# Kernel tuning notes

Hardware: AMD Instinct MI355X
Metric: run time of the kernel (lower is better)

## Reference

```python
import jax, jax.numpy as jnp
import numpy as np

N, B, OBS, ACT = 8, 32768, 128, 32
E, H = 128, 4
D = E // H  # attend_dim = 32
EPS = 1e-5


def setup_inputs() -> dict:
    key = jax.random.key(0)
    ks = jax.random.split(key, 20)
    sc = np.float32(0.02)
    inp = {
        "observation_vector": jax.random.normal(ks[0], (N, B, OBS), jnp.float32),
        "action_vector": jax.random.normal(ks[1], (N, B, ACT), jnp.float32),
        # per-agent BatchNorm affine params (training-mode batch stats are used)
        "bn_g_gamma": jnp.ones((N, OBS + ACT), jnp.float32),
        "bn_g_beta": jnp.zeros((N, OBS + ACT), jnp.float32),
        "bn_s_gamma": jnp.ones((N, OBS), jnp.float32),
        "bn_s_beta": jnp.zeros((N, OBS), jnp.float32),
        # per-agent g / state-only Linear layers
        "g_w": jax.random.normal(ks[2], (N, E, OBS + ACT), jnp.float32) * sc,
        "g_b": jnp.zeros((N, E), jnp.float32),
        "s_w": jax.random.normal(ks[3], (N, E, OBS), jnp.float32) * sc,
        "s_b": jnp.zeros((N, E), jnp.float32),
        # per-head attention projections (no bias)
        "wq": jax.random.normal(ks[4], (H, D, E), jnp.float32) * sc,
        "wk": jax.random.normal(ks[5], (H, D, E), jnp.float32) * sc,
        "wv": jax.random.normal(ks[6], (H, D, E), jnp.float32) * sc,
        # per-agent f networks: Linear(E + H*D -> E), Linear(E -> ACT)
        "f1_w": jax.random.normal(ks[7], (N, E, E + H * D), jnp.float32) * sc,
        "f1_b": jnp.zeros((N, E), jnp.float32),
        "f2_w": jax.random.normal(ks[8], (N, ACT, E), jnp.float32) * sc,
        "f2_b": jnp.zeros((N, ACT), jnp.float32),
    }
    return inp


def _bn(x, gamma, beta):
    # x: [N, B, F]; training-mode BatchNorm1d per agent (biased variance)
    mu = x.mean(axis=1, keepdims=True)
    var = x.var(axis=1, keepdims=True)
    return (x - mu) / jnp.sqrt(var + EPS) * gamma[:, None, :] + beta[:, None, :]


def _lrelu(x):
    return jax.nn.leaky_relu(x, 0.01)


def reference(observation_vector, action_vector, bn_g_gamma, bn_g_beta, bn_s_gamma,
              bn_s_beta, g_w, g_b, s_w, s_b, wq, wk, wv, f1_w, f1_b, f2_w, f2_b):
    obs, act = observation_vector, action_vector
    ga = jnp.concatenate([obs, act], axis=-1)                       # [N,B,OBS+ACT]
    e = _lrelu(jnp.einsum('nbf,nef->nbe', _bn(ga, bn_g_gamma, bn_g_beta), g_w)
               + g_b[:, None, :])                                   # [N,B,E]
    s = _lrelu(jnp.einsum('nbf,nef->nbe', _bn(obs, bn_s_gamma, bn_s_beta), s_w)
               + s_b[:, None, :])                                   # [N,B,E]
    q = jnp.einsum('nbe,hde->hnbd', e, wq)                          # [H,N,B,D]
    k = jnp.einsum('nbe,hde->hnbd', e, wk)
    v = _lrelu(jnp.einsum('nbe,hde->hnbd', e, wv))
    # leave-one-out attention over agents: mask the diagonal (self)
    logits = jnp.einsum('hnbd,hmbd->hbnm', q, k) / jnp.sqrt(jnp.float32(D))
    logits = jnp.where(jnp.eye(N, dtype=bool), -jnp.inf, logits)
    alpha = jax.nn.softmax(logits, axis=-1)                         # [H,B,N,N]
    xi = jnp.einsum('hbnm,hmbd->nbhd', alpha, v)                    # [N,B,H,D]
    xi = xi.reshape(N, xi.shape[1], H * D)
    fin = jnp.concatenate([xi, s], axis=-1)                         # [N,B,H*D+E]
    h1 = _lrelu(jnp.einsum('nbf,nef->nbe', fin, f1_w) + f1_b[:, None, :])
    all_q = jnp.einsum('nbe,nae->nba', h1, f2_w) + f2_b[:, None, :]  # [N,B,ACT]
    ids = jnp.argmax(act, axis=-1, keepdims=True)                   # [N,B,1]
    curr_q = jnp.take_along_axis(all_q, ids, axis=-1)               # [N,B,1]
    return curr_q
```

## Files before the change

### kernel.cpp

```cpp
#include <hip/hip_runtime.h>

#define N_AG 8
#define BTOT 32768
#define OBSF 128
#define ACTF 32
#define HH 4

#define WS_STATS   0u
#define WS_SCALES  (16u<<10)
#define WS_BIASES  (48u<<10)
#define WS_WQKV    (64u<<10)
#define WS_F2W     (160u<<10)
#define WS_F1W     (224u<<10)
#define WS_WG      (768u<<10)
#define WS_IDS     (1536u<<10)
#define WS_ES      (4u<<20)
#define WS_XI      (136u<<20)
#define WS_NEED    ((size_t)200<<20)

typedef __attribute__((ext_vector_type(8))) __bf16 bf16x8;
typedef __attribute__((ext_vector_type(8))) short short8;
typedef __attribute__((ext_vector_type(4))) float f32x4;

static __device__ __forceinline__ unsigned short f2bf(float f){
  unsigned u = __builtin_bit_cast(unsigned, f);
  u += 0x7fffu + ((u >> 16) & 1u);
  return (unsigned short)(u >> 16);
}
static __device__ __forceinline__ bf16x8 ldb8(const unsigned short* p){
  return __builtin_bit_cast(bf16x8, *(const short8*)p);
}
static __device__ __forceinline__ f32x4 mfma16(bf16x8 a, bf16x8 b, f32x4 c){
  return __builtin_amdgcn_mfma_f32_16x16x32_bf16(a, b, c, 0, 0, 0);
}

__global__ void k_zero(float* stats){
  for (int i = threadIdx.x; i < 2560; i += 256) stats[i] = 0.f;
}

__global__ __launch_bounds__(256) void k_stats_obs(const float* __restrict__ obs,
                                                   float* __restrict__ stats){
  int n = blockIdx.y, ch = blockIdx.x;
  int c = threadIdx.x & 31, r = threadIdx.x >> 5;
  const float4* p = (const float4*)(obs + ((size_t)n*BTOT + (size_t)ch*256 + r)*OBSF) + c;
  float sx=0.f, sy=0.f, sz=0.f, sw=0.f;
  float qx=0.f, qy=0.f, qz=0.f, qw=0.f;
  #pragma unroll 4
  for (int i = 0; i < 32; i++){
    float4 v = p[(size_t)i*8*(OBSF/4)];
    sx += v.x; sy += v.y; sz += v.z; sw += v.w;
    qx += v.x*v.x; qy += v.y*v.y; qz += v.z*v.z; qw += v.w*v.w;
  }
  __shared__ float4 rs[8][32], rq[8][32];
  rs[r][c] = make_float4(sx, sy, sz, sw);
  rq[r][c] = make_float4(qx, qy, qz, qw);
  __syncthreads();
  if (threadIdx.x < 128){
    int f = threadIdx.x;
    float ss = 0.f, qq = 0.f;
    #pragma unroll
    for (int g = 0; g < 8; g++){
      ss += ((const float*)&rs[g][f>>2])[f&3];
      qq += ((const float*)&rq[g][f>>2])[f&3];
    }
    atomicAdd(&stats[n*128 + f], ss);
    atomicAdd(&stats[1024 + n*128 + f], qq);
  }
}

__global__ __launch_bounds__(256) void k_stats_act(const float* __restrict__ act,
                                                   float* __restrict__ stats,
                                                   int* __restrict__ ids){
  int n = blockIdx.y, ch = blockIdx.x;
  int c = threadIdx.x & 7, r = threadIdx.x >> 3;
  int f0 = c*4;
  float sx=0.f, sy=0.f, sz=0.f, sw=0.f;
  float qx=0.f, qy=0.f, qz=0.f, qw=0.f;
  #pragma unroll
  for (int i = 0; i < 4; i++){
    int b = ch*128 + i*32 + r;
    float4 v = *(const float4*)(act + ((size_t)n*BTOT + b)*ACTF + f0);
    sx += v.x; sy += v.y; sz += v.z; sw += v.w;
    qx += v.x*v.x; qy += v.y*v.y; qz += v.z*v.z; qw += v.w*v.w;
    float mv = v.x; int mi = f0;
    if (v.y > mv){ mv = v.y; mi = f0+1; }
    if (v.z > mv){ mv = v.z; mi = f0+2; }
    if (v.w > mv){ mv = v.w; mi = f0+3; }
    #pragma unroll
    for (int m = 1; m <= 4; m <<= 1){
      float ov = __shfl_xor(mv, m);
      int   oi = __shfl_xor(mi, m);
      if (ov > mv || (ov == mv && oi < mi)){ mv = ov; mi = oi; }
    }
    if (c == 0) ids[(size_t)n*BTOT + b] = mi;
  }
  __shared__ float4 rs[32][8], rq[32][8];
  rs[r][c] = make_float4(sx, sy, sz, sw);
  rq[r][c] = make_float4(qx, qy, qz, qw);
  __syncthreads();
  if (threadIdx.x < 32){
    int f = threadIdx.x;
    float ss = 0.f, qq = 0.f;
    #pragma unroll
    for (int g = 0; g < 32; g++){
      ss += ((const float*)&rs[g][f>>2])[f&3];
      qq += ((const float*)&rq[g][f>>2])[f&3];
    }
    atomicAdd(&stats[2048 + n*32 + f], ss);
    atomicAdd(&stats[2304 + n*32 + f], qq);
  }
}

__global__ void k_finalize(const float* __restrict__ stats, const float* __restrict__ gg,
                           const float* __restrict__ gb, const float* __restrict__ sg,
                           const float* __restrict__ sb, float* __restrict__ scales){
  int n = blockIdx.x, f = threadIdx.x;
  if (f < 160){
    float mu, va;
    if (f < 128){ mu = stats[n*128+f] * (1.f/BTOT); va = stats[1024+n*128+f]*(1.f/BTOT) - mu*mu; }
    else { int fa = f-128; mu = stats[2048+n*32+fa]*(1.f/BTOT); va = stats[2304+n*32+fa]*(1.f/BTOT) - mu*mu; }
    float inv = 1.f / sqrtf(va + 1e-5f);
    float a = gg[n*160+f] * inv;
    scales[n*160+f] = a;
    scales[1280 + n*160+f] = gb[n*160+f] - mu*a;
    if (f < 128){
      float a2 = sg[n*128+f] * inv;
      scales[2560 + n*128+f] = a2;
      scales[3584 + n*128+f] = sb[n*128+f] - mu*a2;
    }
  }
}

__global__ void k_fold(const float* __restrict__ g_w, const float* __restrict__ g_b,
                       const float* __restrict__ s_w, const float* __restrict__ s_b,
                       const float* __restrict__ wq, const float* __restrict__ wk,
                       const float* __restrict__ wv, const float* __restrict__ f1w_in,
                       const float* __restrict__ f2w_in, const float* __restrict__ scales,
                       unsigned short* __restrict__ wg, float* __restrict__ bias_es,
                       unsigned short* __restrict__ wqkv, unsigned short* __restrict__ f1w,
                       unsigned short* __restrict__ f2w){
  int blk = blockIdx.x, t = threadIdx.x;
  if (blk < 2048){
    int n = blk >> 8, o = blk & 255;
    float part = 0.f;
    if (t < 160){
      float w, a, c;
      if (o < 128){ w = g_w[((size_t)n*128 + o)*160 + t]; a = scales[n*160+t]; c = scales[1280+n*160+t]; }
      else if (t < 128){ w = s_w[((size_t)n*128 + (o-128))*128 + t]; a = scales[2560+n*128+t]; c = scales[3584+n*128+t]; }
      else { w = 0.f; a = 0.f; c = 0.f; }
      wg[((size_t)n*256 + o)*160 + t] = f2bf(w*a);
      part = w * c;
    }
    __shared__ float red[256];
    red[t] = part; __syncthreads();
    for (int s2 = 128; s2 > 0; s2 >>= 1){ if (t < s2) red[t] += red[t+s2]; __syncthreads(); }
    if (t == 0){
      float base = (o < 128) ? g_b[n*128+o] : s_b[n*128+(o-128)];
      bias_es[n*256+o] = base + red[0];
    }
  } else if (blk < 2240){
    int idx = (blk-2048)*256 + t;
    int r = idx >> 7, f = idx & 127, rr = r & 127;
    const float* src = (r < 128) ? wq : (r < 256 ? wk : wv);
    wqkv[idx] = f2bf(src[rr*128 + f]);
  } else if (blk < 3264){
    int idx = (blk-2240)*256 + t;
    f1w[idx] = f2bf(f1w_in[idx]);
  } else {
    int idx = (blk-3264)*256 + t;
    f2w[idx] = f2bf(f2w_in[idx]);
  }
}

__global__ __launch_bounds__(512) void k_gemm_es(const float* __restrict__ obs,
    const float* __restrict__ act, const unsigned short* __restrict__ wg,
    const float* __restrict__ biases, unsigned short* __restrict__ es){
  int n = blockIdx.y, mbb = blockIdx.x;
  int tid = threadIdx.x, w = tid >> 6, l = tid & 63, lr = l & 15, lg = l >> 4;
  __shared__ unsigned short wsm[256*160];
  {
    const int4* src = (const int4*)(wg + (size_t)n*(256*160));
    int4* dst = (int4*)wsm;
    for (int i = tid; i < 256*160/8; i += 512) dst[i] = src[i];
  }
  int brow = mbb*256 + w*16 + lr;
  size_t bglob = (size_t)n*BTOT + brow;
  float4 x0[10];
  #pragma unroll
  for (int kt = 0; kt < 4; kt++){
    const float4* pa = (const float4*)(obs + bglob*OBSF + kt*32 + lg*8);
    x0[kt*2] = pa[0]; x0[kt*2+1] = pa[1];
  }
  { const float4* pa = (const float4*)(act + bglob*ACTF + lg*8);
    x0[8] = pa[0]; x0[9] = pa[1]; }
  __syncthreads();
  f32x4 zero = {0.f,0.f,0.f,0.f};
  bf16x8 af[5];
  #pragma unroll
  for (int kt = 0; kt < 5; kt++){
    float4 a = x0[kt*2], b = x0[kt*2+1];
    af[kt][0]=(__bf16)a.x; af[kt][1]=(__bf16)a.y; af[kt][2]=(__bf16)a.z; af[kt][3]=(__bf16)a.w;
    af[kt][4]=(__bf16)b.x; af[kt][5]=(__bf16)b.y; af[kt][6]=(__bf16)b.z; af[kt][7]=(__bf16)b.w;
  }
  float4 x1[10];
  #pragma unroll
  for (int kt = 0; kt < 4; kt++){
    const float4* pa = (const float4*)(obs + (bglob+128)*OBSF + kt*32 + lg*8);
    x1[kt*2] = pa[0]; x1[kt*2+1] = pa[1];
  }
  { const float4* pa = (const float4*)(act + (bglob+128)*ACTF + lg*8);
    x1[8] = pa[0]; x1[9] = pa[1]; }
  f32x4 acc[16];
  #pragma unroll
  for (int i = 0; i < 16; i++) acc[i] = zero;
  #pragma unroll
  for (int kt = 0; kt < 5; kt++)
    #pragma unroll
    for (int nt = 0; nt < 16; nt++){
      bf16x8 bf = ldb8(&wsm[(nt*16 + lr)*160 + kt*32 + lg*8]);
      acc[nt] = mfma16(af[kt], bf, acc[nt]);
    }
  #pragma unroll
  for (int nt = 0; nt < 16; nt++){
    int col = nt*16 + lr;
    float bias = biases[n*256 + col];
    #pragma unroll
    for (int r = 0; r < 4; r++){
      float v = acc[nt][r] + bias;
      v = v > 0.f ? v : 0.01f*v;
      int orow = mbb*256 + w*16 + lg*4 + r;
      es[((size_t)n*BTOT + orow)*256 + col] = f2bf(v);
    }
  }
  #pragma unroll
  for (int kt = 0; kt < 5; kt++){
    float4 a = x1[kt*2], b = x1[kt*2+1];
    af[kt][0]=(__bf16)a.x; af[kt][1]=(__bf16)a.y; af[kt][2]=(__bf16)a.z; af[kt][3]=(__bf16)a.w;
    af[kt][4]=(__bf16)b.x; af[kt][5]=(__bf16)b.y; af[kt][6]=(__bf16)b.z; af[kt][7]=(__bf16)b.w;
  }
  #pragma unroll
  for (int i = 0; i < 16; i++) acc[i] = zero;
  #pragma unroll
  for (int kt = 0; kt < 5; kt++)
    #pragma unroll
    for (int nt = 0; nt < 16; nt++){
      bf16x8 bf = ldb8(&wsm[(nt*16 + lr)*160 + kt*32 + lg*8]);
      acc[nt] = mfma16(af[kt], bf, acc[nt]);
    }
  #pragma unroll
  for (int nt = 0; nt < 16; nt++){
    int col = nt*16 + lr;
    float bias = biases[n*256 + col];
    #pragma unroll
    for (int r = 0; r < 4; r++){
      float v = acc[nt][r] + bias;
      v = v > 0.f ? v : 0.01f*v;
      int orow = mbb*256 + 128 + w*16 + lg*4 + r;
      es[((size_t)n*BTOT + orow)*256 + col] = f2bf(v);
    }
  }
}

__global__ __launch_bounds__(256) void k_attn(const unsigned short* __restrict__ es,
    const unsigned short* __restrict__ wqkv, unsigned short* __restrict__ xi){
  int bt = blockIdx.x;
  int tid = threadIdx.x, w = tid >> 6, l = tid & 63, lr = l & 15, lg = l >> 4;
  __shared__ unsigned short qkvT[128][104];
  bf16x8 e0[4], e1[4];
  {
    int r0 = w*32 + lr, r1 = r0 + 16;
    const unsigned short* p0 = &es[((size_t)(r0>>4)*BTOT + bt*16 + (r0&15))*256];
    const unsigned short* p1 = &es[((size_t)(r1>>4)*BTOT + bt*16 + (r1&15))*256];
    #pragma unroll
    for (int kt = 0; kt < 4; kt++){
      e0[kt] = ldb8(p0 + kt*32 + lg*8);
      e1[kt] = ldb8(p1 + kt*32 + lg*8);
    }
  }
  #pragma unroll
  for (int h = 0; h < HH; h++){
    f32x4 zero = {0.f,0.f,0.f,0.f};
    f32x4 acc[2][6];
    #pragma unroll
    for (int mt = 0; mt < 2; mt++)
      #pragma unroll
      for (int nt = 0; nt < 6; nt++) acc[mt][nt] = zero;
    #pragma unroll
    for (int kt = 0; kt < 4; kt++){
      int f0 = kt*32 + lg*8;
      #pragma unroll
      for (int nt = 0; nt < 6; nt++){
        int r = nt*16 + lr, sec = r >> 5, j = r & 31;
        bf16x8 bf = ldb8(&wqkv[((size_t)sec*128 + h*32 + j)*128 + f0]);
        acc[0][nt] = mfma16(e0[kt], bf, acc[0][nt]);
        acc[1][nt] = mfma16(e1[kt], bf, acc[1][nt]);
      }
    }
    __syncthreads();
    #pragma unroll
    for (int mt = 0; mt < 2; mt++)
      #pragma unroll
      for (int nt = 0; nt < 6; nt++)
        #pragma unroll
        for (int r = 0; r < 4; r++){
          float v = acc[mt][nt][r];
          if (nt >= 4) v = v > 0.f ? v : 0.01f*v;
          qkvT[w*32 + mt*16 + lg*4 + r][nt*16 + lr] = f2bf(v);
        }
    __syncthreads();
    {
      int dh = tid & 1, bi = (tid >> 1) & 15, nq = tid >> 5;
      int rq = nq*16 + bi;
      float qv[16];
      { bf16x8 t0 = ldb8(&qkvT[rq][dh*16]);
        bf16x8 t1 = ldb8(&qkvT[rq][dh*16 + 8]);
        #pragma unroll
        for (int i = 0; i < 8; i++){ qv[i] = (float)t0[i]; qv[8+i] = (float)t1[i]; } }
      float lgt[8];
      #pragma unroll
      for (int m = 0; m < 8; m++){
        bf16x8 k0 = ldb8(&qkvT[m*16+bi][32 + dh*16]);
        bf16x8 k1 = ldb8(&qkvT[m*16+bi][32 + dh*16 + 8]);
        float d = 0.f;
        #pragma unroll
        for (int i = 0; i < 8; i++){ d += qv[i]*(float)k0[i]; d += qv[8+i]*(float)k1[i]; }
        d += __shfl_xor(d, 1);
        lgt[m] = d * 0.17677669529663687f;
      }
      float mx = -1e30f;
      #pragma unroll
      for (int m = 0; m < 8; m++) if (m != nq) mx = fmaxf(mx, lgt[m]);
      float p[8], sum = 0.f;
      #pragma unroll
      for (int m = 0; m < 8; m++){ p[m] = (m == nq) ? 0.f : __expf(lgt[m] - mx); sum += p[m]; }
      float inv = 1.f / sum;
      float xa[16];
      #pragma unroll
      for (int i = 0; i < 16; i++) xa[i] = 0.f;
      #pragma unroll
      for (int m = 0; m < 8; m++){
        float al = p[m]*inv;
        bf16x8 v0 = ldb8(&qkvT[m*16+bi][64 + dh*16]);
        bf16x8 v1 = ldb8(&qkvT[m*16+bi][64 + dh*16 + 8]);
        #pragma unroll
        for (int i = 0; i < 8; i++){ xa[i] += al*(float)v0[i]; xa[8+i] += al*(float)v1[i]; }
      }
      short8 o0, o1;
      #pragma unroll
      for (int i = 0; i < 8; i++){ o0[i] = (short)f2bf(xa[i]); o1[i] = (short)f2bf(xa[8+i]); }
      size_t orow = (size_t)nq*BTOT + bt*16 + bi;
      *(short8*)&xi[orow*128 + h*32 + dh*16]     = o0;
      *(short8*)&xi[orow*128 + h*32 + dh*16 + 8] = o1;
    }
  }
}

__global__ __launch_bounds__(512) void k_gemm_f(const unsigned short* __restrict__ xi,
    const unsigned short* __restrict__ es, const unsigned short* __restrict__ f1w,
    const float* __restrict__ f1b, const unsigned short* __restrict__ f2w,
    const float* __restrict__ f2b, const int* __restrict__ ids,
    float* __restrict__ out){
  int n = blockIdx.y, mbb = blockIdx.x;
  int tid = threadIdx.x, w = tid >> 6, l = tid & 63, lr = l & 15, lg = l >> 4;
  __shared__ unsigned short f1T[128*264];
  __shared__ unsigned short f2T[32*136];
  __shared__ unsigned short h1T[128*136];
  __shared__ float allq[128*32];
  for (int i = tid; i < 128*32; i += 512){
    int r = i >> 5, c = (i & 31)*8;
    *(int4*)&f1T[r*264 + c] = *(const int4*)&f1w[((size_t)n*128 + r)*256 + c];
  }
  for (int i = tid; i < 32*16; i += 512){
    int r = i >> 4, c = (i & 15)*8;
    *(int4*)&f2T[r*136 + c] = *(const int4*)&f2w[((size_t)n*32 + r)*128 + c];
  }
  bf16x8 xf[2][8];
  {
    int arow0 = mbb*256 + w*16 + lr;
    #pragma unroll
    for (int kt = 0; kt < 4; kt++)
      xf[0][kt] = ldb8(&xi[((size_t)n*BTOT + arow0)*128 + kt*32 + lg*8]);
    #pragma unroll
    for (int kt = 0; kt < 4; kt++)
      xf[0][4+kt] = ldb8(&es[((size_t)n*BTOT + arow0)*256 + 128 + kt*32 + lg*8]);
  }
  __syncthreads();
  f32x4 zero = {0.f,0.f,0.f,0.f};
  #pragma unroll
  for (int sub = 0; sub < 2; sub++){
    const int cur = sub & 1, nxt = cur ^ 1;
    int mb = mbb*2 + sub;
    int arow = mb*128 + w*16 + lr;
    if (sub < 1){
      int arown = arow + 128;
      #pragma unroll
      for (int kt = 0; kt < 4; kt++)
        xf[nxt][kt] = ldb8(&xi[((size_t)n*BTOT + arown)*128 + kt*32 + lg*8]);
      #pragma unroll
      for (int kt = 0; kt < 4; kt++)
        xf[nxt][4+kt] = ldb8(&es[((size_t)n*BTOT + arown)*256 + 128 + kt*32 + lg*8]);
    }
    f32x4 a1[8];
    #pragma unroll
    for (int i = 0; i < 8; i++) a1[i] = zero;
    #pragma unroll
    for (int kt = 0; kt < 8; kt++)
      #pragma unroll
      for (int nt = 0; nt < 8; nt++){
        bf16x8 bf = ldb8(&f1T[(nt*16 + lr)*264 + kt*32 + lg*8]);
        a1[nt] = mfma16(xf[cur][kt], bf, a1[nt]);
      }
    #pragma unroll
    for (int nt = 0; nt < 8; nt++){
      int col = nt*16 + lr;
      float bias = f1b[n*128 + col];
      #pragma unroll
      for (int r = 0; r < 4; r++){
        float v = a1[nt][r] + bias;
        v = v > 0.f ? v : 0.01f*v;
        h1T[(w*16 + lg*4 + r)*136 + col] = f2bf(v);
      }
    }
    __syncthreads();
    f32x4 a2[2];
    a2[0] = zero; a2[1] = zero;
    #pragma unroll
    for (int kt = 0; kt < 4; kt++){
      int f0 = kt*32 + lg*8;
      bf16x8 hf = ldb8(&h1T[(w*16 + lr)*136 + f0]);
      #pragma unroll
      for (int nt = 0; nt < 2; nt++){
        bf16x8 bf = ldb8(&f2T[(nt*16 + lr)*136 + f0]);
        a2[nt] = mfma16(hf, bf, a2[nt]);
      }
    }
    #pragma unroll
    for (int nt = 0; nt < 2; nt++){
      int col = nt*16 + lr;
      float bias = f2b[n*32 + col];
      #pragma unroll
      for (int r = 0; r < 4; r++)
        allq[(w*16 + lg*4 + r)*32 + col] = a2[nt][r] + bias;
    }
    __syncthreads();
    if (tid < 128){
      size_t bglob = (size_t)mb*128 + tid;
      int id = ids[(size_t)n*BTOT + bglob];
      out[(size_t)n*BTOT + bglob] = allq[tid*32 + id];
    }
  }
}

extern "C" void kernel_launch(void* const* d_in, const int* in_sizes, int n_in,
                              void* d_out, int out_size, void* d_ws, size_t ws_size,
                              hipStream_t stream){
  if (ws_size < WS_NEED) return;
  const float* obs  = (const float*)d_in[0];
  const float* act  = (const float*)d_in[1];
  const float* gg   = (const float*)d_in[2];
  const float* gb   = (const float*)d_in[3];
  const float* sg   = (const float*)d_in[4];
  const float* sb   = (const float*)d_in[5];
  const float* g_w  = (const float*)d_in[6];
  const float* g_b  = (const float*)d_in[7];
  const float* s_w  = (const float*)d_in[8];
  const float* s_b  = (const float*)d_in[9];
  const float* wq   = (const float*)d_in[10];
  const float* wk   = (const float*)d_in[11];
  const float* wv   = (const float*)d_in[12];
  const float* f1w_in = (const float*)d_in[13];
  const float* f1b  = (const float*)d_in[14];
  const float* f2w_in = (const float*)d_in[15];
  const float* f2b  = (const float*)d_in[16];
  char* ws = (char*)d_ws;
  float* stats   = (float*)(ws + WS_STATS);
  float* scales  = (float*)(ws + WS_SCALES);
  float* bias_es = (float*)(ws + WS_BIASES);
  unsigned short* wqkv = (unsigned short*)(ws + WS_WQKV);
  unsigned short* f2wb = (unsigned short*)(ws + WS_F2W);
  unsigned short* f1wb = (unsigned short*)(ws + WS_F1W);
  unsigned short* wg   = (unsigned short*)(ws + WS_WG);
  int* ids             = (int*)(ws + WS_IDS);
  unsigned short* esb  = (unsigned short*)(ws + WS_ES);
  unsigned short* xib  = (unsigned short*)(ws + WS_XI);
  float* out = (float*)d_out;

  k_zero<<<1, 256, 0, stream>>>(stats);
  k_stats_obs<<<dim3(128,8), 256, 0, stream>>>(obs, stats);
  k_stats_act<<<dim3(256,8), 256, 0, stream>>>(act, stats, ids);
  k_finalize<<<8, 256, 0, stream>>>(stats, gg, gb, sg, sb, scales);
  k_fold<<<3392, 256, 0, stream>>>(g_w, g_b, s_w, s_b, wq, wk, wv, f1w_in, f2w_in,
                                   scales, wg, bias_es, wqkv, f1wb, f2wb);
  k_gemm_es<<<dim3(128,8), 512, 0, stream>>>(obs, act, wg, bias_es, esb);
  k_attn<<<2048, 256, 0, stream>>>(esb, wqkv, xib);
  k_gemm_f<<<dim3(128,8), 512, 0, stream>>>(xib, esb, f1wb, f1b, f2wb, f2b, ids, out);
}
```

Baseline: 299.4 us.

## Split attention into separate QKV projection GEMM and attention-scores kernel

The fused attention kernel, which computed Q/K/V per head with weights read from global memory and staged them in LDS, is split in two. A new GEMM kernel computes all 384 Q/K/V columns per agent with the weights held in LDS and writes them to a bf16 global buffer. A second kernel reads Q/K/V back from global memory to do the leave-one-out softmax attention. This trades extra global traffic (about 200MB written and read) for a more efficient projection GEMM with weight reuse, and it doubles the workspace requirement.

```diff
diff --git a/kernel.cpp b/kernel.cpp
--- a/kernel.cpp
+++ b/kernel.cpp
@@ -16,7 +16,8 @@
 #define WS_IDS     (1536u<<10)
 #define WS_ES      (4u<<20)
 #define WS_XI      (136u<<20)
-#define WS_NEED    ((size_t)200<<20)
+#define WS_QKV     (200u<<20)
+#define WS_NEED    ((size_t)400<<20)
 
 typedef __attribute__((ext_vector_type(8))) __bf16 bf16x8;
 typedef __attribute__((ext_vector_type(8))) short short8;
@@ -261,97 +262,99 @@
   }
 }
 
-__global__ __launch_bounds__(256) void k_attn(const unsigned short* __restrict__ es,
-    const unsigned short* __restrict__ wqkv, unsigned short* __restrict__ xi){
+__global__ __launch_bounds__(512) void k_qkv(const unsigned short* __restrict__ es,
+    const unsigned short* __restrict__ wqkv, unsigned short* __restrict__ qkvg){
+  int n = blockIdx.y, mbb = blockIdx.x;
+  int tid = threadIdx.x, w = tid >> 6, l = tid & 63, lr = l & 15, lg = l >> 4;
+  __shared__ unsigned short wsm[384*132];
+  for (int i = tid; i < 384*16; i += 512){
+    int r = i >> 4, c = (i & 15)*8;
+    *(int4*)&wsm[r*132 + c] = *(const int4*)&wqkv[(size_t)r*128 + c];
+  }
+  __syncthreads();
+  f32x4 zero = {0.f,0.f,0.f,0.f};
+  #pragma unroll
+  for (int sub = 0; sub < 2; sub++){
+    int row = mbb*256 + sub*128 + w*16 + lr;
+    bf16x8 af[4];
+    #pragma unroll
+    for (int kt = 0; kt < 4; kt++)
+      af[kt] = ldb8(&es[((size_t)n*BTOT + row)*256 + kt*32 + lg*8]);
+    f32x4 acc[24];
+    #pragma unroll
+    for (int i = 0; i < 24; i++) acc[i] = zero;
+    #pragma unroll
+    for (int kt = 0; kt < 4; kt++)
+      #pragma unroll
+      for (int nt = 0; nt < 24; nt++){
+        bf16x8 bf = ldb8(&wsm[(nt*16 + lr)*132 + kt*32 + lg*8]);
+        acc[nt] = mfma16(af[kt], bf, acc[nt]);
+      }
+    #pragma unroll
+    for (int nt = 0; nt < 24; nt++){
+      int col = nt*16 + lr;
+      #pragma unroll
+      for (int r = 0; r < 4; r++){
+        float v = acc[nt][r];
+        if (nt >= 16) v = v > 0.f ? v : 0.01f*v;
+        int orow = mbb*256 + sub*128 + w*16 + lg*4 + r;
+        qkvg[((size_t)n*BTOT + orow)*384 + col] = f2bf(v);
+      }
+    }
+  }
+}
+
+__global__ __launch_bounds__(256) void k_attnsc(const unsigned short* __restrict__ qkvg,
+    unsigned short* __restrict__ xi){
   int bt = blockIdx.x;
-  int tid = threadIdx.x, w = tid >> 6, l = tid & 63, lr = l & 15, lg = l >> 4;
-  __shared__ unsigned short qkvT[128][104];
-  bf16x8 e0[4], e1[4];
-  {
-    int r0 = w*32 + lr, r1 = r0 + 16;
-    const unsigned short* p0 = &es[((size_t)(r0>>4)*BTOT + bt*16 + (r0&15))*256];
-    const unsigned short* p1 = &es[((size_t)(r1>>4)*BTOT + bt*16 + (r1&15))*256];
-    #pragma unroll
-    for (int kt = 0; kt < 4; kt++){
-      e0[kt] = ldb8(p0 + kt*32 + lg*8);
-      e1[kt] = ldb8(p1 + kt*32 + lg*8);
-    }
-  }
+  int tid = threadIdx.x;
+  int dh = tid & 1, bi = (tid >> 1) & 15, nq = tid >> 5;
+  int b = bt*16 + bi;
   #pragma unroll
   for (int h = 0; h < HH; h++){
-    f32x4 zero = {0.f,0.f,0.f,0.f};
-    f32x4 acc[2][6];
-    #pragma unroll
-    for (int mt = 0; mt < 2; mt++)
-      #pragma unroll
-      for (int nt = 0; nt < 6; nt++) acc[mt][nt] = zero;
-    #pragma unroll
-    for (int kt = 0; kt < 4; kt++){
-      int f0 = kt*32 + lg*8;
-      #pragma unroll
-      for (int nt = 0; nt < 6; nt++){
-        int r = nt*16 + lr, sec = r >> 5, j = r & 31;
-        bf16x8 bf = ldb8(&wqkv[((size_t)sec*128 + h*32 + j)*128 + f0]);
-        acc[0][nt] = mfma16(e0[kt], bf, acc[0][nt]);
-        acc[1][nt] = mfma16(e1[kt], bf, acc[1][nt]);
-      }
-    }
-    __syncthreads();
-    #pragma unroll
-    for (int mt = 0; mt < 2; mt++)
-      #pragma unroll
-      for (int nt = 0; nt < 6; nt++)
-        #pragma unroll
-        for (int r = 0; r < 4; r++){
-          float v = acc[mt][nt][r];
-          if (nt >= 4) v = v > 0.f ? v : 0.01f*v;
-          qkvT[w*32 + mt*16 + lg*4 + r][nt*16 + lr] = f2bf(v);
-        }
-    __syncthreads();
-    {
-      int dh = tid & 1, bi = (tid >> 1) & 15, nq = tid >> 5;
-      int rq = nq*16 + bi;
-      float qv[16];
-      { bf16x8 t0 = ldb8(&qkvT[rq][dh*16]);
-        bf16x8 t1 = ldb8(&qkvT[rq][dh*16 + 8]);
-        #pragma unroll
-        for (int i = 0; i < 8; i++){ qv[i] = (float)t0[i]; qv[8+i] = (float)t1[i]; } }
-      float lgt[8];
-      #pragma unroll
-      for (int m = 0; m < 8; m++){
-        bf16x8 k0 = ldb8(&qkvT[m*16+bi][32 + dh*16]);
-        bf16x8 k1 = ldb8(&qkvT[m*16+bi][32 + dh*16 + 8]);
-        float d = 0.f;
-        #pragma unroll
-        for (int i = 0; i < 8; i++){ d += qv[i]*(float)k0[i]; d += qv[8+i]*(float)k1[i]; }
-        d += __shfl_xor(d, 1);
-        lgt[m] = d * 0.17677669529663687f;
-      }
-      float mx = -1e30f;
-      #pragma unroll
-      for (int m = 0; m < 8; m++) if (m != nq) mx = fmaxf(mx, lgt[m]);
-      float p[8], sum = 0.f;
-      #pragma unroll
-      for (int m = 0; m < 8; m++){ p[m] = (m == nq) ? 0.f : __expf(lgt[m] - mx); sum += p[m]; }
-      float inv = 1.f / sum;
-      float xa[16];
-      #pragma unroll
-      for (int i = 0; i < 16; i++) xa[i] = 0.f;
-      #pragma unroll
-      for (int m = 0; m < 8; m++){
-        float al = p[m]*inv;
-        bf16x8 v0 = ldb8(&qkvT[m*16+bi][64 + dh*16]);
-        bf16x8 v1 = ldb8(&qkvT[m*16+bi][64 + dh*16 + 8]);
-        #pragma unroll
-        for (int i = 0; i < 8; i++){ xa[i] += al*(float)v0[i]; xa[8+i] += al*(float)v1[i]; }
-      }
-      short8 o0, o1;
-      #pragma unroll
-      for (int i = 0; i < 8; i++){ o0[i] = (short)f2bf(xa[i]); o1[i] = (short)f2bf(xa[8+i]); }
-      size_t orow = (size_t)nq*BTOT + bt*16 + bi;
-      *(short8*)&xi[orow*128 + h*32 + dh*16]     = o0;
-      *(short8*)&xi[orow*128 + h*32 + dh*16 + 8] = o1;
-    }
+    float qv[16];
+    { const unsigned short* qp = &qkvg[((size_t)nq*BTOT + b)*384 + h*32 + dh*16];
+      bf16x8 t0 = ldb8(qp);
+      bf16x8 t1 = ldb8(qp + 8);
+      #pragma unroll
+      for (int i = 0; i < 8; i++){ qv[i] = (float)t0[i]; qv[8+i] = (float)t1[i]; } }
+    float lgt[8];
+    #pragma unroll
+    for (int m = 0; m < 8; m++){
+      const unsigned short* kp = &qkvg[((size_t)m*BTOT + b)*384 + 128 + h*32 + dh*16];
+      bf16x8 k0 = ldb8(kp);
+      bf16x8 k1 = ldb8(kp + 8);
+      float d = 0.f;
+      #pragma unroll
+      for (int i = 0; i < 8; i++){ d += qv[i]*(float)k0[i]; d += qv[8+i]*(float)k1[i]; }
+      d += __shfl_xor(d, 1);
+      lgt[m] = d * 0.17677669529663687f;
+    }
+    float mx = -1e30f;
+    #pragma unroll
+    for (int m = 0; m < 8; m++) if (m != nq) mx = fmaxf(mx, lgt[m]);
+    float p[8], sum = 0.f;
+    #pragma unroll
+    for (int m = 0; m < 8; m++){ p[m] = (m == nq) ? 0.f : __expf(lgt[m] - mx); sum += p[m]; }
+    float inv = 1.f / sum;
+    float xa[16];
+    #pragma unroll
+    for (int i = 0; i < 16; i++) xa[i] = 0.f;
+    #pragma unroll
+    for (int m = 0; m < 8; m++){
+      float al = p[m]*inv;
+      const unsigned short* vp = &qkvg[((size_t)m*BTOT + b)*384 + 256 + h*32 + dh*16];
+      bf16x8 v0 = ldb8(vp);
+      bf16x8 v1 = ldb8(vp + 8);
+      #pragma unroll
+      for (int i = 0; i < 8; i++){ xa[i] += al*(float)v0[i]; xa[8+i] += al*(float)v1[i]; }
+    }
+    short8 o0, o1;
+    #pragma unroll
+    for (int i = 0; i < 8; i++){ o0[i] = (short)f2bf(xa[i]); o1[i] = (short)f2bf(xa[8+i]); }
+    size_t orow = (size_t)nq*BTOT + b;
+    *(short8*)&xi[orow*128 + h*32 + dh*16]     = o0;
+    *(short8*)&xi[orow*128 + h*32 + dh*16 + 8] = o1;
   }
 }
 
@@ -483,6 +486,7 @@
   int* ids             = (int*)(ws + WS_IDS);
   unsigned short* esb  = (unsigned short*)(ws + WS_ES);
   unsigned short* xib  = (unsigned short*)(ws + WS_XI);
+  unsigned short* qkvg = (unsigned short*)(ws + WS_QKV);
   float* out = (float*)d_out;
 
   k_zero<<<1, 256, 0, stream>>>(stats);
@@ -492,6 +496,7 @@
   k_fold<<<3392, 256, 0, stream>>>(g_w, g_b, s_w, s_b, wq, wk, wv, f1w_in, f2w_in,
                                    scales, wg, bias_es, wqkv, f1wb, f2wb);
   k_gemm_es<<<dim3(128,8), 512, 0, stream>>>(obs, act, wg, bias_es, esb);
-  k_attn<<<2048, 256, 0, stream>>>(esb, wqkv, xib);
+  k_qkv<<<dim3(128,8), 512, 0, stream>>>(esb, wqkv, qkvg);
+  k_attnsc<<<2048, 256, 0, stream>>>(qkvg, xib);
   k_gemm_f<<<dim3(128,8), 512, 0, stream>>>(xib, esb, f1wb, f1b, f2wb, f2b, ids, out);
 }
```

New measurement: 491.6 us. 64.2% more time.
